# Optimization experiments

Measured on AMD Instinct MI355X. Metric: run time of the kernel, lower is better.

## Reference

```python
import jax, jax.numpy as jnp
import numpy as np

N_NODES = 100000
N_EDGES = 1600000
D = 128  # in_features


def setup_inputs() -> dict:
    key = jax.random.key(0)
    k1, k2, k3 = jax.random.split(key, 3)
    node_embeddings = jax.random.normal(k1, (N_NODES, D), dtype=jnp.float32)
    edge_index = jax.random.randint(k2, (2, N_EDGES), 0, N_NODES, dtype=jnp.int64)
    # attn_fc: Linear(2*D, 2) -> weight [2, 2*D], bias [2]
    W = jax.random.normal(k3, (2, 2 * D), dtype=jnp.float32) * (1.0 / np.sqrt(2 * D))
    b = jnp.zeros((2,), dtype=jnp.float32)
    return {"node_embeddings": node_embeddings, "edge_index": edge_index, "W": W, "b": b}


def reference(node_embeddings, edge_index, W, b):
    # Gather endpoint embeddings per edge, concat -> [E, 2*D]
    row, col = edge_index[0], edge_index[1]
    edge_feature = jnp.concatenate(
        [node_embeddings[row], node_embeddings[col]], axis=-1
    )  # [E, 2D]
    attn_scores = edge_feature @ W.T + b  # [E, 2]
    attn_scores = jax.nn.softmax(attn_scores, axis=-1)
    # dropout is identity in eval mode
    return attn_scores
```

## Files before the change

### kernel.cpp

```cpp
#include <hip/hip_runtime.h>

static constexpr int kNodes = 100000;
static constexpr int kEdges = 1600000;
static constexpr int kD     = 128;

__global__ __launch_bounds__(64) void detect_idx(const unsigned long long* __restrict__ ei,
                                                 int* __restrict__ flag) {
    if (threadIdx.x == 0 && blockIdx.x == 0) {
        unsigned long long orr = 0ull;
        for (int i = 0; i < 256; ++i) orr |= (ei[i] >> 32);
        *flag = (orr == 0ull) ? 1 : 0;
    }
}

__global__ __launch_bounds__(256) void node_pre(const float* __restrict__ emb,
                                                const float* __restrict__ W,
                                                float* __restrict__ h) {
    const int lane16 = threadIdx.x & 15;
    const int c0 = lane16 * 8;

    float w0[8], w1[8], w2[8], w3[8];
#pragma unroll
    for (int k = 0; k < 8; ++k) {
        w0[k] = W[c0 + k];
        w1[k] = W[256 + c0 + k];
        w2[k] = W[128 + c0 + k];
        w3[k] = W[384 + c0 + k];
    }

    const int group   = (blockIdx.x * blockDim.x + threadIdx.x) >> 4;
    const int ngroups = (gridDim.x * blockDim.x) >> 4;

    for (int n = group; n < kNodes; n += ngroups) {
        const float4* row = (const float4*)(emb + (size_t)n * kD + c0);
        float4 ea = row[0];
        float4 eb = row[1];
        float e[8] = {ea.x, ea.y, ea.z, ea.w, eb.x, eb.y, eb.z, eb.w};
        float p0 = 0.f, p1 = 0.f, p2 = 0.f, p3 = 0.f;
#pragma unroll
        for (int k = 0; k < 8; ++k) {
            p0 += e[k] * w0[k];
            p1 += e[k] * w1[k];
            p2 += e[k] * w2[k];
            p3 += e[k] * w3[k];
        }
#pragma unroll
        for (int m = 1; m < 16; m <<= 1) {
            p0 += __shfl_xor(p0, m, 64);
            p1 += __shfl_xor(p1, m, 64);
            p2 += __shfl_xor(p2, m, 64);
            p3 += __shfl_xor(p3, m, 64);
        }
        if (lane16 == 0) {
            ((float4*)h)[n] = make_float4(p0, p1, p2, p3);
        }
    }
}

__global__ __launch_bounds__(256) void edge_attn(const void* __restrict__ eiv,
                                                 const float* __restrict__ h,
                                                 const float* __restrict__ b,
                                                 const int* __restrict__ flag,
                                                 float* __restrict__ out) {
    const int e = blockIdx.x * blockDim.x + threadIdx.x;
    if (e >= kEdges) return;

    int r, c;
    if (*flag) {
        const long long* ei = (const long long*)eiv;
        r = (int)ei[e];
        c = (int)ei[kEdges + e];
    } else {
        const int* ei = (const int*)eiv;
        r = ei[e];
        c = ei[kEdges + e];
    }

    float4 hr = ((const float4*)h)[r];
    float4 hc = ((const float4*)h)[c];

    const float b0 = b[0], b1 = b[1];
    float s0 = hr.x + hc.z + b0;
    float s1 = hr.y + hc.w + b1;
    float m  = fmaxf(s0, s1);
    float x0 = __expf(s0 - m);
    float x1 = __expf(s1 - m);
    float inv = 1.0f / (x0 + x1);
    ((float2*)out)[e] = make_float2(x0 * inv, x1 * inv);
}

extern "C" void kernel_launch(void* const* d_in, const int* in_sizes, int n_in,
                              void* d_out, int out_size, void* d_ws, size_t ws_size,
                              hipStream_t stream) {
    const float* emb = (const float*)d_in[0];
    const void*  ei  = d_in[1];
    const float* W   = (const float*)d_in[2];
    const float* b   = (const float*)d_in[3];
    float* out = (float*)d_out;

    int*   flag = (int*)d_ws;
    float* h    = (float*)((char*)d_ws + 256);

    detect_idx<<<1, 64, 0, stream>>>((const unsigned long long*)ei, flag);

    node_pre<<<(kNodes * 16 + 255) / 256, 256, 0, stream>>>(emb, W, h);

    edge_attn<<<(kEdges + 255) / 256, 256, 0, stream>>>(ei, h, b, flag, out);
}
```

Baseline: 36.88 us.

## Inline index-width detection, drop detect kernel, process two edges per thread

```diff
diff --git a/kernel.cpp b/kernel.cpp
--- a/kernel.cpp
+++ b/kernel.cpp
@@ -3,15 +3,6 @@
 static constexpr int kNodes = 100000;
 static constexpr int kEdges = 1600000;
 static constexpr int kD     = 128;
-
-__global__ __launch_bounds__(64) void detect_idx(const unsigned long long* __restrict__ ei,
-                                                 int* __restrict__ flag) {
-    if (threadIdx.x == 0 && blockIdx.x == 0) {
-        unsigned long long orr = 0ull;
-        for (int i = 0; i < 256; ++i) orr |= (ei[i] >> 32);
-        *flag = (orr == 0ull) ? 1 : 0;
-    }
-}
 
 __global__ __launch_bounds__(256) void node_pre(const float* __restrict__ emb,
                                                 const float* __restrict__ W,
@@ -28,65 +19,81 @@
         w3[k] = W[384 + c0 + k];
     }
 
-    const int group   = (blockIdx.x * blockDim.x + threadIdx.x) >> 4;
-    const int ngroups = (gridDim.x * blockDim.x) >> 4;
+    const int n = (blockIdx.x * blockDim.x + threadIdx.x) >> 4;
+    if (n >= kNodes) return;
 
-    for (int n = group; n < kNodes; n += ngroups) {
-        const float4* row = (const float4*)(emb + (size_t)n * kD + c0);
-        float4 ea = row[0];
-        float4 eb = row[1];
-        float e[8] = {ea.x, ea.y, ea.z, ea.w, eb.x, eb.y, eb.z, eb.w};
-        float p0 = 0.f, p1 = 0.f, p2 = 0.f, p3 = 0.f;
+    const float4* row = (const float4*)(emb + (size_t)n * kD + c0);
+    float4 ea = row[0];
+    float4 eb = row[1];
+    float e[8] = {ea.x, ea.y, ea.z, ea.w, eb.x, eb.y, eb.z, eb.w};
+    float p0 = 0.f, p1 = 0.f, p2 = 0.f, p3 = 0.f;
 #pragma unroll
-        for (int k = 0; k < 8; ++k) {
-            p0 += e[k] * w0[k];
-            p1 += e[k] * w1[k];
-            p2 += e[k] * w2[k];
-            p3 += e[k] * w3[k];
-        }
+    for (int k = 0; k < 8; ++k) {
+        p0 += e[k] * w0[k];
+        p1 += e[k] * w1[k];
+        p2 += e[k] * w2[k];
+        p3 += e[k] * w3[k];
+    }
 #pragma unroll
-        for (int m = 1; m < 16; m <<= 1) {
-            p0 += __shfl_xor(p0, m, 64);
-            p1 += __shfl_xor(p1, m, 64);
-            p2 += __shfl_xor(p2, m, 64);
-            p3 += __shfl_xor(p3, m, 64);
-        }
-        if (lane16 == 0) {
-            ((float4*)h)[n] = make_float4(p0, p1, p2, p3);
-        }
+    for (int m = 1; m < 16; m <<= 1) {
+        p0 += __shfl_xor(p0, m, 64);
+        p1 += __shfl_xor(p1, m, 64);
+        p2 += __shfl_xor(p2, m, 64);
+        p3 += __shfl_xor(p3, m, 64);
+    }
+    if (lane16 == 0) {
+        ((float4*)h)[n] = make_float4(p0, p1, p2, p3);
     }
 }
 
 __global__ __launch_bounds__(256) void edge_attn(const void* __restrict__ eiv,
                                                  const float* __restrict__ h,
                                                  const float* __restrict__ b,
-                                                 const int* __restrict__ flag,
                                                  float* __restrict__ out) {
-    const int e = blockIdx.x * blockDim.x + threadIdx.x;
-    if (e >= kEdges) return;
+    const unsigned long long* ei64 = (const unsigned long long*)eiv;
+    unsigned long long hi = ei64[threadIdx.x & 63] >> 32;
+    const bool is64 = (__ballot(hi != 0ull) == 0ull);
 
-    int r, c;
-    if (*flag) {
-        const long long* ei = (const long long*)eiv;
-        r = (int)ei[e];
-        c = (int)ei[kEdges + e];
+    const int e2 = blockIdx.x * blockDim.x + threadIdx.x;
+    if (e2 >= kEdges / 2) return;
+
+    int r0, r1, c0, c1;
+    if (is64) {
+        ulonglong2 rr = ((const ulonglong2*)ei64)[e2];
+        ulonglong2 cc = ((const ulonglong2*)(ei64 + kEdges))[e2];
+        r0 = (int)rr.x; r1 = (int)rr.y;
+        c0 = (int)cc.x; c1 = (int)cc.y;
     } else {
-        const int* ei = (const int*)eiv;
-        r = ei[e];
-        c = ei[kEdges + e];
+        const int* ei32 = (const int*)eiv;
+        int2 rr = ((const int2*)ei32)[e2];
+        int2 cc = ((const int2*)(ei32 + kEdges))[e2];
+        r0 = rr.x; r1 = rr.y;
+        c0 = cc.x; c1 = cc.y;
     }
 
-    float4 hr = ((const float4*)h)[r];
-    float4 hc = ((const float4*)h)[c];
+    const float4* h4 = (const float4*)h;
+    float4 hr0 = h4[r0];
+    float4 hc0 = h4[c0];
+    float4 hr1 = h4[r1];
+    float4 hc1 = h4[c1];
 
     const float b0 = b[0], b1 = b[1];
-    float s0 = hr.x + hc.z + b0;
-    float s1 = hr.y + hc.w + b1;
-    float m  = fmaxf(s0, s1);
-    float x0 = __expf(s0 - m);
-    float x1 = __expf(s1 - m);
-    float inv = 1.0f / (x0 + x1);
-    ((float2*)out)[e] = make_float2(x0 * inv, x1 * inv);
+
+    float s00 = hr0.x + hc0.z + b0;
+    float s01 = hr0.y + hc0.w + b1;
+    float m0  = fmaxf(s00, s01);
+    float x00 = __expf(s00 - m0);
+    float x01 = __expf(s01 - m0);
+    float i0  = 1.0f / (x00 + x01);
+
+    float s10 = hr1.x + hc1.z + b0;
+    float s11 = hr1.y + hc1.w + b1;
+    float m1  = fmaxf(s10, s11);
+    float x10 = __expf(s10 - m1);
+    float x11 = __expf(s11 - m1);
+    float i1  = 1.0f / (x10 + x11);
+
+    ((float4*)out)[e2] = make_float4(x00 * i0, x01 * i0, x10 * i1, x11 * i1);
 }
 
 extern "C" void kernel_launch(void* const* d_in, const int* in_sizes, int n_in,
@@ -98,12 +105,9 @@
     const float* b   = (const float*)d_in[3];
     float* out = (float*)d_out;
 
-    int*   flag = (int*)d_ws;
-    float* h    = (float*)((char*)d_ws + 256);
-
-    detect_idx<<<1, 64, 0, stream>>>((const unsigned long long*)ei, flag);
+    float* h = (float*)d_ws;
 
     node_pre<<<(kNodes * 16 + 255) / 256, 256, 0, stream>>>(emb, W, h);
 
-    edge_attn<<<(kEdges + 255) / 256, 256, 0, stream>>>(ei, h, b, flag, out);
+    edge_attn<<<(kEdges / 2 + 255) / 256, 256, 0, stream>>>(ei, h, b, out);
 }
```

Result: faster. 32.76 us (-11.2%).
